# Optimization experiments

Hardware: AMD Instinct MI355X
Metric: run time of the kernel (lower is better)

## Reference

```python
import jax, jax.numpy as jnp
import numpy as np

B, S, D, H = 2, 2048, 2048, 16
HD = D // H  # head dim = 128


def setup_inputs() -> dict:
    key = jax.random.key(0)
    ks = jax.random.split(key, 9)
    sc = 1.0 / np.sqrt(D)
    return {
        "hidden_states": jax.random.normal(ks[0], (B, S, D), jnp.float32),
        "Wq": jax.random.normal(ks[1], (D, D), jnp.float32) * sc,
        "bq": jax.random.normal(ks[2], (D,), jnp.float32) * 0.02,
        "Wk": jax.random.normal(ks[3], (D, D), jnp.float32) * sc,
        "bk": jax.random.normal(ks[4], (D,), jnp.float32) * 0.02,
        "Wv": jax.random.normal(ks[5], (D, D), jnp.float32) * sc,
        "bv": jax.random.normal(ks[6], (D,), jnp.float32) * 0.02,
        "Wo": jax.random.normal(ks[7], (D, D), jnp.float32) * sc,
        "bo": jax.random.normal(ks[8], (D,), jnp.float32) * 0.02,
    }


def _rotate_half(x):
    x1, x2 = jnp.split(x, 2, axis=-1)
    return jnp.concatenate((-x2, x1), axis=-1)


def reference(hidden_states, Wq, bq, Wk, bk, Wv, bv, Wo, bo):
    b, s, d = hidden_states.shape
    # QKV projections (torch Linear: x @ W.T + b)
    def proj(W, bias):
        y = jnp.einsum('bsd,ed->bse', hidden_states, W) + bias
        return y.reshape(b, s, H, HD).transpose(0, 2, 1, 3)  # [B,H,S,HD]
    q, k, v = proj(Wq, bq), proj(Wk, bk), proj(Wv, bv)

    # Rotary embedding tables
    inv_freq = 1.0 / (10000.0 ** (jnp.arange(0, HD, 2, dtype=jnp.float32) / HD))
    t = jnp.arange(s, dtype=jnp.float32)
    freqs = jnp.einsum('i,j->ij', t, inv_freq)          # [S, HD/2]
    emb = jnp.concatenate((freqs, freqs), axis=-1)       # [S, HD]
    cos_cached, sin_cached = jnp.cos(emb), jnp.sin(emb)
    # NOTE: source unpacks `sin, cos = rotary_emb(...)` while forward returns
    # (cos, sin) -> swap is intentional to match original math.
    sin_t, cos_t = cos_cached, sin_cached
    q = q * cos_t + _rotate_half(q) * sin_t
    k = k * cos_t + _rotate_half(k) * sin_t

    scores = jnp.einsum('bhsd,bhtd->bhst', q, k) / jnp.sqrt(jnp.float32(HD))
    probs = jax.nn.softmax(scores, axis=-1)
    ctx = jnp.einsum('bhst,bhtd->bhsd', probs, v)
    ctx = ctx.transpose(0, 2, 1, 3).reshape(b, s, d)
    return jnp.einsum('bsd,ed->bse', ctx, Wo) + bo
```

## Files before the change

### kernel.cpp

```cpp
#include <hip/hip_runtime.h>

constexpr int NH = 16;
constexpr int SEQ = 2048;
constexpr int DMODEL = 2048;
constexpr int HDIM = 128;
constexpr int NB = 2;
constexpr int MTOT = NB * SEQ;
constexpr long NEL = (long)NB * SEQ * DMODEL;
constexpr long WEL = (long)DMODEL * DMODEL;
constexpr size_t FUSED_WS = 2ul * (4 * NEL + 3 * WEL + 12288);

typedef __attribute__((ext_vector_type(8))) __bf16 bf16x8;
typedef __attribute__((ext_vector_type(4))) float f32x4;

__device__ __forceinline__ float bf2f(ushort u) {
  union { uint i; float f; } v; v.i = ((uint)u) << 16; return v.f;
}
__device__ __forceinline__ ushort f2bf(float f) {
  union { float f; uint i; } v; v.f = f;
  uint r = (v.i + 0x7FFFu + ((v.i >> 16) & 1u)) >> 16;
  return (ushort)r;
}
__device__ __forceinline__ ushort f2bf_rhu(float f) {
  union { float f; uint i; } v; v.f = f;
  return (ushort)((v.i + 0x8000u) >> 16);
}
__device__ __forceinline__ float fast_exp2(float x) {
#if __has_builtin(__builtin_amdgcn_exp2f)
  return __builtin_amdgcn_exp2f(x);
#else
  float r;
  asm volatile("v_exp_f32 %0, %1\n\ts_nop 0" : "=v"(r) : "v"(x));
  return r;
#endif
}

__global__ __launch_bounds__(256) void conv_f32_bf16(
    const float* __restrict__ s, ushort* __restrict__ d, int n4) {
  const int i = blockIdx.x * 256 + threadIdx.x;
  if (i < n4) {
    const float4 v = ((const float4*)s)[i];
    ushort4 o;
    o.x = f2bf(v.x); o.y = f2bf(v.y); o.z = f2bf(v.z); o.w = f2bf(v.w);
    ((ushort4*)d)[i] = o;
  }
}

__global__ __launch_bounds__(256) void bias_cat(
    const float* __restrict__ a, const float* __restrict__ b,
    const float* __restrict__ c, float* __restrict__ o) {
  const int i = blockIdx.x * 256 + threadIdx.x;
  o[i] = (i < 2048) ? a[i] : (i < 4096) ? b[i - 2048] : c[i - 4096];
}

#define GLDS(src, dst)                                              \
  __builtin_amdgcn_global_load_lds(                                 \
      (const __attribute__((address_space(1))) void*)(src),         \
      (__attribute__((address_space(3))) void*)(dst), 16, 0, 0)

#define STG_A(d, kt) do {                                           \
    const ushort* _s = gA + (long)(kt) * 64;                        \
    ushort* _d = smem + (d) * 8192 + w * 512;                       \
    GLDS(_s, _d);                                                   \
    GLDS(_s + 64 * (long)K, _d + 4096);                             \
  } while (0)

#define STG_B0(d, kt) do {                                          \
    const ushort* _s = gB + (long)(kt) * 64;                        \
    ushort* _d = smem + 16384 + (d) * 16384 + w * 512;              \
    GLDS(_s, _d);                                                   \
    GLDS(_s + 64 * (long)K, _d + 4096);                             \
  } while (0)

#define STG_B1(d, kt) do {                                          \
    const ushort* _s = gB + 128 * (long)K + (long)(kt) * 64;        \
    ushort* _d = smem + 16384 + (d) * 16384 + 8192 + w * 512;       \
    GLDS(_s, _d);                                                   \
    GLDS(_s + 64 * (long)K, _d + 4096);                             \
  } while (0)

#define LDAF(d) do {                                                \
    const ushort* _p = smem + (d) * 8192 + (wm * 64 + l16) * 64;    \
    _Pragma("unroll")                                               \
    for (int _i = 0; _i < 4; _i++) {                                \
      afr[_i][0] = *(const bf16x8*)(_p + _i * 1024 + sw0);          \
      afr[_i][1] = *(const bf16x8*)(_p + _i * 1024 + sw1);          \
    }                                                               \
  } while (0)

#define LDBF(d, nh) do {                                            \
    const ushort* _p = smem + 16384 + (d) * 16384 +                 \
                       ((nh) * 128 + wn * 32 + l16) * 64;           \
    _Pragma("unroll")                                               \
    for (int _j = 0; _j < 2; _j++) {                                \
      bfr[nh][_j][0] = *(const bf16x8*)(_p + _j * 1024 + sw0);      \
      bfr[nh][_j][1] = *(const bf16x8*)(_p + _j * 1024 + sw1);      \
    }                                                               \
  } while (0)

#define MMAP(nh) do {                                               \
    __builtin_amdgcn_s_setprio(1);                                  \
    _Pragma("unroll")                                               \
    for (int _i = 0; _i < 4; _i++)                                  \
      _Pragma("unroll")                                             \
      for (int _j = 0; _j < 2; _j++) {                              \
        acc[_i][(nh) * 2 + _j] = __builtin_amdgcn_mfma_f32_16x16x32_bf16( \
            afr[_i][0], bfr[nh][_j][0], acc[_i][(nh) * 2 + _j], 0, 0, 0); \
        acc[_i][(nh) * 2 + _j] = __builtin_amdgcn_mfma_f32_16x16x32_bf16( \
            afr[_i][1], bfr[nh][_j][1], acc[_i][(nh) * 2 + _j], 0, 0, 0); \
      }                                                             \
    __builtin_amdgcn_s_setprio(0);                                  \
  } while (0)

#define BARX() __builtin_amdgcn_s_barrier()
#define WAITV(n) asm volatile("s_waitcnt vmcnt(" #n ")" ::: "memory")
#define WAITL() asm volatile("s_waitcnt lgkmcnt(0)" ::: "memory")

template <int MODE>
__global__ __launch_bounds__(512, 2) void gemm128(
    const ushort* __restrict__ A, const ushort* __restrict__ Bw,
    const float* __restrict__ bias, void* __restrict__ Cv,
    int M, int N, int K) {
  __shared__ __align__(16) ushort smem[49152];
  const int tid = threadIdx.x;
  const int w = tid >> 6, lane = tid & 63;
  const int quad = lane >> 4, l16 = lane & 15;
  const int wm = w >> 2, wn = w & 3;
  const int nbm = M >> 7, nbn = N >> 8;
  const int rm = nbm >> 1, rn = nbn >> 2;
  const int xcd = blockIdx.x & 7, loc = blockIdx.x >> 3;
  const int bm = (xcd >> 2) * rm + (loc % rm);
  const int bn = (xcd & 3) * rn + (loc / rm);
  const int m0 = bm << 7, n0 = bn << 8;
  const int KT = K >> 6;

  const int srow = tid >> 3;
  const int scol = (((tid & 7) ^ ((tid >> 3) & 7)) << 3);
  const ushort* gA = A + (long)(m0 + srow) * K + scol;
  const ushort* gB = Bw + (long)(n0 + srow) * K + scol;
  const int sw0 = ((quad ^ (l16 & 7)) << 3);
  const int sw1 = (((4 + quad) ^ (l16 & 7)) << 3);

  f32x4 acc[4][4] = {};
  bf16x8 afr[4][2];
  bf16x8 bfr[2][2][2];

  STG_B1(0, 0);
  STG_A(0, 0); STG_B0(0, 0);
  STG_A(1, 1); STG_B0(1, 1);
  WAITV(4);
  BARX();
  LDAF(0); LDBF(0, 0);
  WAITL();
  BARX();

  for (int t = 0; t < KT; t++) {
    const int d = t & 1, nd = d ^ 1;
    const int c1 = (t + 1 < KT) ? t + 1 : 0;
    const int c2 = (t + 2 < KT) ? t + 2 : (t + 2 - KT);
    STG_B1(nd, c1);
    STG_A(d, c2);
    WAITV(8);
    BARX();
    WAITL();
    MMAP(0);
    LDBF(d, 1);
    BARX();
    STG_B0(d, c2);
    WAITV(6);
    BARX();
    WAITL();
    MMAP(1);
    LDAF(nd); LDBF(nd, 0);
    BARX();
  }

#pragma unroll
  for (int i = 0; i < 4; i++) {
    const int rbase = m0 + wm * 64 + i * 16 + quad * 4;
#pragma unroll
    for (int nh = 0; nh < 2; nh++)
#pragma unroll
      for (int j = 0; j < 2; j++) {
        const int col = n0 + nh * 128 + wn * 32 + j * 16 + l16;
        const float bv = bias[col];
#pragma unroll
        for (int r = 0; r < 4; r++) {
          const int row = rbase + r;
          const float v = acc[i][nh * 2 + j][r] + bv;
          if (MODE == 0) {
            ((float*)Cv)[(long)row * N + col] = v;
          } else {
            const int b = row >> 11, s = row & (SEQ - 1);
            const int h = (col >> 7) & 15, hd = col & (HDIM - 1);
            const long off = (long)(col >> 11) * NEL +
                ((long)(b * NH + h) * SEQ + s) * HDIM + hd;
            ((ushort*)Cv)[off] = f2bf(v);
          }
        }
      }
  }
}

__global__ __launch_bounds__(256) void rope_qk(ushort* Q, ushort* Kt) {
  const int gid = blockIdx.x * 256 + threadIdx.x;
  const int n = gid & 4194303;
  const bool isK = (gid >= 4194304);
  ushort* ptr = isK ? Kt : Q;
  const float qs = isK ? 1.0f : 0.12751743f;
  const int p = n & 63;
  const int s = (n >> 6) & (SEQ - 1);
  const int bh = n >> 17;
  const long idx = (long)bh * (SEQ * HDIM) + (long)s * HDIM + p;
  const float invf_rev =
      fast_exp2(-(float)p * 0.2076205059304601f) * 0.15915494309189535f;
  float rev = (float)s * invf_rev;
  rev -= floorf(rev);
  const float sn = __builtin_amdgcn_sinf(rev);
  const float cs = __builtin_amdgcn_cosf(rev);
  const float x1 = bf2f(ptr[idx]);
  const float x2 = bf2f(ptr[idx + 64]);
  ptr[idx]      = f2bf((x1 * sn - x2 * cs) * qs);
  ptr[idx + 64] = f2bf((x2 * sn + x1 * cs) * qs);
}

__global__ __launch_bounds__(256) void transpose_v(const ushort* __restrict__ V,
                                                   ushort* __restrict__ VT) {
  __shared__ ushort lT[64 * 65];
  const int bh = blockIdx.x >> 6;
  const int rem = blockIdx.x & 63;
  const int t0 = (rem >> 1) << 6, d0 = (rem & 1) << 6;
  const ushort* vb = V + (long)bh * (SEQ * HDIM);
  ushort* ob = VT + (long)bh * (SEQ * HDIM);
  const int tid = threadIdx.x;
#pragma unroll
  for (int it = 0; it < 16; it++) {
    const int idx = it * 256 + tid;
    const int r = idx >> 6, c = idx & 63;
    lT[c * 65 + r] = vb[(long)(t0 + r) * HDIM + d0 + c];
  }
  __syncthreads();
#pragma unroll
  for (int it = 0; it < 16; it++) {
    const int idx = it * 256 + tid;
    const int r = idx >> 6, c = idx & 63;
    ob[(long)(d0 + r) * SEQ + t0 + c] = lT[r * 65 + c];
  }
}

__global__ __launch_bounds__(256, 2) void attn(const ushort* __restrict__ Q,
                                               const ushort* __restrict__ Kp,
                                               const ushort* __restrict__ VT,
                                               ushort* __restrict__ ctx) {
  __shared__ __align__(16) ushort smem[40960];
  const int tid = threadIdx.x;
  const int wave = tid >> 6, lane = tid & 63;
  const int quad = lane >> 4, l16 = lane & 15;
  const int xcd = blockIdx.x & 7, loc = blockIdx.x >> 3;
  const int bh = xcd * 4 + (loc >> 5), qt = loc & 31;
  const long hb = (long)bh * (SEQ * HDIM);
  const int b = bh >> 4, h = bh & 15;
  const int qh = wave & 1, th = wave >> 1;
  ushort* myP = smem + 35840 + wave * (32 * 40);

  bf16x8 qa[2][4];
#pragma unroll
  for (int qq = 0; qq < 2; qq++)
#pragma unroll
    for (int c = 0; c < 4; c++)
      qa[qq][c] = *(const bf16x8*)(
          Q + hb + (long)(qt * 64 + qh * 32 + qq * 16 + l16) * HDIM +
          c * 32 + (quad << 3));

  f32x4 o[2][8] = {};
  f32x4 lacc[2] = {};
  bf16x8 ones;
#pragma unroll
  for (int i = 0; i < 8; i++) ones[i] = (__bf16)1.0f;

  const ushort* kSrc = Kp + hb + (long)(tid >> 4) * HDIM + (tid & 15) * 8;
  const ushort* vSrc = VT + hb + (long)(tid >> 3) * SEQ + (tid & 7) * 8;
  const int kOff = (tid >> 4) * 136 + (tid & 15) * 8;
  const int vOff = (tid >> 3) * 72 + (tid & 7) * 8;

  {
    bf16x8 kR[4], vR[4];
#pragma unroll
    for (int it = 0; it < 4; it++) {
      kR[it] = *(const bf16x8*)(kSrc + (long)it * (16 * HDIM));
      vR[it] = *(const bf16x8*)(vSrc + (long)it * (32 * SEQ));
    }
    kSrc += 64 * HDIM; vSrc += 64;
#pragma unroll
    for (int it = 0; it < 4; it++) {
      *(bf16x8*)(smem + kOff + it * (16 * 136)) = kR[it];
      *(bf16x8*)(smem + 17408 + vOff + it * (32 * 72)) = vR[it];
    }
  }
  __syncthreads();

  for (int t0 = 0; t0 < SEQ; t0 += 64) {
    const int cur = (t0 >> 6) & 1;
    ushort* cK = cur ? smem + 8704 : smem;
    ushort* cV = cur ? smem + 26624 : smem + 17408;
    ushort* nK = cur ? smem : smem + 8704;
    ushort* nV = cur ? smem + 17408 : smem + 26624;
    const bool more = (t0 + 64 < SEQ);

    bf16x8 kR[4], vR[4];
    if (more) {
#pragma unroll
      for (int it = 0; it < 4; it++) {
        kR[it] = *(const bf16x8*)(kSrc + (long)it * (16 * HDIM));
        vR[it] = *(const bf16x8*)(vSrc + (long)it * (32 * SEQ));
      }
      kSrc += 64 * HDIM; vSrc += 64;
    }

    const ushort* kRow = cK + (th * 32 + l16) * 136 + (quad << 3);
    f32x4 st[2][2] = {};
    __builtin_amdgcn_s_setprio(1);
#pragma unroll
    for (int kc = 0; kc < 4; kc++)
#pragma unroll
      for (int tt = 0; tt < 2; tt++) {
        const bf16x8 ka = *(const bf16x8*)(kRow + tt * (16 * 136) + kc * 32);
#pragma unroll
        for (int qq = 0; qq < 2; qq++)
          st[tt][qq] = __builtin_amdgcn_mfma_f32_16x16x32_bf16(
              ka, qa[qq][kc], st[tt][qq], 0, 0, 0);
      }
    __builtin_amdgcn_s_setprio(0);

    ushort* pW = myP + l16 * 40 + (quad << 2);
#pragma unroll
    for (int qq = 0; qq < 2; qq++)
#pragma unroll
      for (int tt = 0; tt < 2; tt++) {
        ushort4 pk;
        pk.x = f2bf_rhu(fast_exp2(st[tt][qq][0]));
        pk.y = f2bf_rhu(fast_exp2(st[tt][qq][1]));
        pk.z = f2bf_rhu(fast_exp2(st[tt][qq][2]));
        pk.w = f2bf_rhu(fast_exp2(st[tt][qq][3]));
        *(ushort4*)(pW + qq * (16 * 40) + tt * 16) = pk;
      }
    WAITL();
    __builtin_amdgcn_sched_barrier(0);

    const ushort* pRow = myP + l16 * 40 + (quad << 3);
    const ushort* vRow = cV + l16 * 72 + th * 32 + (quad << 3);
    bf16x8 pa[2];
    __builtin_amdgcn_s_setprio(1);
#pragma unroll
    for (int qq = 0; qq < 2; qq++) {
      pa[qq] = *(const bf16x8*)(pRow + qq * (16 * 40));
      lacc[qq] = __builtin_amdgcn_mfma_f32_16x16x32_bf16(
          pa[qq], ones, lacc[qq], 0, 0, 0);
    }
#pragma unroll
    for (int nt = 0; nt < 8; nt++) {
      const bf16x8 vb = *(const bf16x8*)(vRow + nt * (16 * 72));
#pragma unroll
      for (int qq = 0; qq < 2; qq++)
        o[qq][nt] = __builtin_amdgcn_mfma_f32_16x16x32_bf16(
            pa[qq], vb, o[qq][nt], 0, 0, 0);
    }
    __builtin_amdgcn_s_setprio(0);

    if (more) {
#pragma unroll
      for (int it = 0; it < 4; it++) {
        *(bf16x8*)(nK + kOff + it * (16 * 136)) = kR[it];
        *(bf16x8*)(nV + vOff + it * (32 * 72)) = vR[it];
      }
    }
    __syncthreads();
  }

  float* mb = (float*)smem;
  if (wave >= 2) {
    float* p = mb + ((wave - 2) * 64 + lane) * 73;
#pragma unroll
    for (int qq = 0; qq < 2; qq++) {
#pragma unroll
      for (int nt = 0; nt < 8; nt++)
#pragma unroll
        for (int r = 0; r < 4; r++) p[qq * 32 + nt * 4 + r] = o[qq][nt][r];
#pragma unroll
      for (int r = 0; r < 4; r++) p[64 + qq * 4 + r] = lacc[qq][r];
    }
  }
  __syncthreads();
  if (wave < 2) {
    const float* p = mb + (wave * 64 + lane) * 73;
#pragma unroll
    for (int qq = 0; qq < 2; qq++) {
#pragma unroll
      for (int nt = 0; nt < 8; nt++)
#pragma unroll
        for (int r = 0; r < 4; r++) o[qq][nt][r] += p[qq * 32 + nt * 4 + r];
#pragma unroll
      for (int r = 0; r < 4; r++) lacc[qq][r] += p[64 + qq * 4 + r];
    }
#pragma unroll
    for (int qq = 0; qq < 2; qq++)
#pragma unroll
      for (int r = 0; r < 4; r++) {
        const float inv = 1.0f / lacc[qq][r];
        const int s = qt * 64 + qh * 32 + qq * 16 + quad * 4 + r;
        const long base = ((long)(b * SEQ + s)) * DMODEL + h * HDIM;
#pragma unroll
        for (int nt = 0; nt < 8; nt++)
          ctx[base + nt * 16 + l16] = f2bf(o[qq][nt][r] * inv);
      }
  }
}

extern "C" void kernel_launch(void* const* d_in, const int* in_sizes, int n_in,
                              void* d_out, int out_size, void* d_ws, size_t ws_size,
                              hipStream_t stream) {
  const float* hid = (const float*)d_in[0];
  const float* Wq = (const float*)d_in[1];
  const float* bq = (const float*)d_in[2];
  const float* Wk = (const float*)d_in[3];
  const float* bk = (const float*)d_in[4];
  const float* Wv = (const float*)d_in[5];
  const float* bv = (const float*)d_in[6];
  const float* Wo = (const float*)d_in[7];
  const float* bo = (const float*)d_in[8];
  float* out = (float*)d_out;
  ushort* ws = (ushort*)d_ws;

  ushort* qw   = ws;
  ushort* kw   = ws + NEL;
  ushort* vw   = ws + 2 * NEL;
  ushort* hidB = ws + 3 * NEL;
  ushort* wB   = ws + 4 * NEL;

  dim3 blk(256);
  dim3 blkG(512);
  conv_f32_bf16<<<(int)(NEL / 4 / 256), blk, 0, stream>>>(hid, hidB, NEL / 4);

  if (ws_size >= FUSED_WS) {
    conv_f32_bf16<<<(int)(WEL / 4 / 256), blk, 0, stream>>>(Wq, wB, WEL / 4);
    conv_f32_bf16<<<(int)(WEL / 4 / 256), blk, 0, stream>>>(Wk, wB + WEL, WEL / 4);
    conv_f32_bf16<<<(int)(WEL / 4 / 256), blk, 0, stream>>>(Wv, wB + 2 * WEL, WEL / 4);
    float* bc = (float*)(wB + 3 * WEL);
    bias_cat<<<24, blk, 0, stream>>>(bq, bk, bv, bc);
    gemm128<1><<<768, blkG, 0, stream>>>(hidB, wB, bc, qw, MTOT, 3 * DMODEL, DMODEL);
  } else {
    conv_f32_bf16<<<(int)(WEL / 4 / 256), blk, 0, stream>>>(Wq, wB, WEL / 4);
    gemm128<1><<<256, blkG, 0, stream>>>(hidB, wB, bq, qw, MTOT, DMODEL, DMODEL);
    conv_f32_bf16<<<(int)(WEL / 4 / 256), blk, 0, stream>>>(Wk, wB, WEL / 4);
    gemm128<1><<<256, blkG, 0, stream>>>(hidB, wB, bk, kw, MTOT, DMODEL, DMODEL);
    conv_f32_bf16<<<(int)(WEL / 4 / 256), blk, 0, stream>>>(Wv, wB, WEL / 4);
    gemm128<1><<<256, blkG, 0, stream>>>(hidB, wB, bv, vw, MTOT, DMODEL, DMODEL);
  }

  rope_qk<<<32768, blk, 0, stream>>>(qw, kw);

  ushort* vtw = hidB;
  transpose_v<<<2048, blk, 0, stream>>>(vw, vtw);

  ushort* cw = vw;
  attn<<<1024, blk, 0, stream>>>(qw, kw, vtw, cw);

  conv_f32_bf16<<<(int)(WEL / 4 / 256), blk, 0, stream>>>(Wo, wB, WEL / 4);
  gemm128<0><<<256, blkG, 0, stream>>>(cw, wB, bo, out, MTOT, DMODEL, DMODEL);
}
```

Measured before the change: 423.1 us.

## Add 128x384-tile GEMM kernel for fused QKV projection

Adds a new gemm384 kernel that computes a 128x384 output tile per block, staging three 128-column B sub-tiles through a 64 KB shared-memory pipeline. The fused QKV projection now launches 512 blocks of it instead of 768 blocks of the 128x256 kernel. The larger N tile is meant to reuse each A tile across more columns and cut global/LDS traffic for A. In exchange it uses more LDS and more accumulator registers per block, which may lower occupancy, and it relies on a more complex interleaved load/MMA schedule.

```diff
diff --git a/kernel.cpp b/kernel.cpp
--- a/kernel.cpp
+++ b/kernel.cpp
@@ -57,6 +57,162 @@
   __builtin_amdgcn_global_load_lds(                                 \
       (const __attribute__((address_space(1))) void*)(src),         \
       (__attribute__((address_space(3))) void*)(dst), 16, 0, 0)
+
+#define BARX() __builtin_amdgcn_s_barrier()
+#define WAITV(n) asm volatile("s_waitcnt vmcnt(" #n ")" ::: "memory")
+#define WAITL() asm volatile("s_waitcnt lgkmcnt(0)" ::: "memory")
+
+#define G3_STG_A(d, kt) do {                                        \
+    const ushort* _s = gA + (long)(kt) * 64;                        \
+    ushort* _d = smem + (d) * 8192 + w * 512;                       \
+    GLDS(_s, _d);                                                   \
+    GLDS(_s + 64 * (long)K, _d + 4096);                             \
+  } while (0)
+
+#define G3_STG_B(d, j, kt) do {                                     \
+    const ushort* _s = gB + (long)(j) * 128 * K + (long)(kt) * 64;  \
+    ushort* _d = smem + 16384 + (d) * 24576 + (j) * 8192 + w * 512; \
+    GLDS(_s, _d);                                                   \
+    GLDS(_s + 64 * (long)K, _d + 4096);                             \
+  } while (0)
+
+#define G3_LDA(d) do {                                              \
+    const ushort* _p = smem + (d) * 8192 + (wm * 64 + l16) * 64;    \
+    _Pragma("unroll")                                               \
+    for (int _i = 0; _i < 4; _i++) {                                \
+      afr[_i][0] = *(const bf16x8*)(_p + _i * 1024 + sw0);          \
+      afr[_i][1] = *(const bf16x8*)(_p + _i * 1024 + sw1);          \
+    }                                                               \
+  } while (0)
+
+#define G3_LDB(d, j, s) do {                                        \
+    const ushort* _p = smem + 16384 + (d) * 24576 + (j) * 8192 +    \
+                       (wn * 32 + l16) * 64;                        \
+    _Pragma("unroll")                                               \
+    for (int _j = 0; _j < 2; _j++) {                                \
+      bfr[s][_j][0] = *(const bf16x8*)(_p + _j * 1024 + sw0);       \
+      bfr[s][_j][1] = *(const bf16x8*)(_p + _j * 1024 + sw1);       \
+    }                                                               \
+  } while (0)
+
+#define G3_MMA(s, j) do {                                           \
+    __builtin_amdgcn_s_setprio(1);                                  \
+    _Pragma("unroll")                                               \
+    for (int _i = 0; _i < 4; _i++)                                  \
+      _Pragma("unroll")                                             \
+      for (int _j = 0; _j < 2; _j++) {                              \
+        acc[_i][(j) * 2 + _j] = __builtin_amdgcn_mfma_f32_16x16x32_bf16( \
+            afr[_i][0], bfr[s][_j][0], acc[_i][(j) * 2 + _j], 0, 0, 0);  \
+        acc[_i][(j) * 2 + _j] = __builtin_amdgcn_mfma_f32_16x16x32_bf16( \
+            afr[_i][1], bfr[s][_j][1], acc[_i][(j) * 2 + _j], 0, 0, 0);  \
+      }                                                             \
+    __builtin_amdgcn_s_setprio(0);                                  \
+  } while (0)
+
+template <int MODE>
+__global__ __launch_bounds__(512, 2) void gemm384(
+    const ushort* __restrict__ A, const ushort* __restrict__ Bw,
+    const float* __restrict__ bias, void* __restrict__ Cv,
+    int M, int N, int K) {
+  __shared__ __align__(16) ushort smem[65536];
+  const int tid = threadIdx.x;
+  const int w = tid >> 6, lane = tid & 63;
+  const int quad = lane >> 4, l16 = lane & 15;
+  const int wm = w >> 2, wn = w & 3;
+  const int nbm = M >> 7, nbn = N / 384;
+  const int rm = nbm >> 1, rn = nbn >> 2;
+  const int xcd = blockIdx.x & 7, loc = blockIdx.x >> 3;
+  const int bm = (xcd >> 2) * rm + (loc % rm);
+  const int bn = (xcd & 3) * rn + (loc / rm);
+  const int m0 = bm << 7, n0 = bn * 384;
+  const int KT = K >> 6;
+
+  const int srow = tid >> 3;
+  const int scol = (((tid & 7) ^ ((tid >> 3) & 7)) << 3);
+  const ushort* gA = A + (long)(m0 + srow) * K + scol;
+  const ushort* gB = Bw + (long)(n0 + srow) * K + scol;
+  const int sw0 = ((quad ^ (l16 & 7)) << 3);
+  const int sw1 = (((4 + quad) ^ (l16 & 7)) << 3);
+
+  f32x4 acc[4][6] = {};
+  bf16x8 afr[4][2];
+  bf16x8 bfr[2][2][2];
+
+  G3_STG_A(0, 0);
+  G3_STG_B(0, 0, 0); G3_STG_B(0, 1, 0); G3_STG_B(0, 2, 0);
+  G3_STG_A(1, 1);
+  G3_STG_B(1, 0, 1); G3_STG_B(1, 1, 1);
+  WAITV(10);
+  BARX();
+  G3_LDA(0); G3_LDB(0, 0, 0);
+  WAITL();
+  BARX();
+
+  for (int t = 0; t < KT; t += 2) {
+    const int e2 = (t + 2 < KT) ? t + 2 : 0;
+    const int e3 = (t + 3 < KT) ? t + 3 : 1;
+    G3_STG_B(1, 2, t + 1);
+    G3_STG_A(0, e2);
+    WAITV(10); BARX(); WAITL();
+    G3_MMA(0, 0);
+    G3_LDB(0, 1, 1);
+    BARX();
+    G3_STG_B(0, 0, e2);
+    BARX(); WAITL();
+    G3_MMA(1, 1);
+    G3_LDB(0, 2, 0);
+    BARX();
+    G3_STG_B(0, 1, e2);
+    WAITV(10); BARX(); WAITL();
+    G3_MMA(0, 2);
+    G3_LDA(1);
+    G3_LDB(1, 0, 1);
+    BARX();
+    G3_STG_B(0, 2, e2);
+    G3_STG_A(1, e3);
+    WAITV(10); BARX(); WAITL();
+    G3_MMA(1, 0);
+    G3_LDB(1, 1, 0);
+    BARX();
+    G3_STG_B(1, 0, e3);
+    BARX(); WAITL();
+    G3_MMA(0, 1);
+    G3_LDB(1, 2, 1);
+    BARX();
+    G3_STG_B(1, 1, e3);
+    WAITV(10); BARX(); WAITL();
+    G3_MMA(1, 2);
+    G3_LDA(0);
+    G3_LDB(0, 0, 0);
+    BARX();
+  }
+
+#pragma unroll
+  for (int i = 0; i < 4; i++) {
+    const int rbase = m0 + wm * 64 + i * 16 + quad * 4;
+#pragma unroll
+    for (int jt = 0; jt < 3; jt++)
+#pragma unroll
+      for (int j = 0; j < 2; j++) {
+        const int col = n0 + jt * 128 + wn * 32 + j * 16 + l16;
+        const float bv = bias[col];
+#pragma unroll
+        for (int r = 0; r < 4; r++) {
+          const int row = rbase + r;
+          const float v = acc[i][jt * 2 + j][r] + bv;
+          if (MODE == 0) {
+            ((float*)Cv)[(long)row * N + col] = v;
+          } else {
+            const int b = row >> 11, s = row & (SEQ - 1);
+            const int h = (col >> 7) & 15, hd = col & (HDIM - 1);
+            const long off = (long)(col >> 11) * NEL +
+                ((long)(b * NH + h) * SEQ + s) * HDIM + hd;
+            ((ushort*)Cv)[off] = f2bf(v);
+          }
+        }
+      }
+  }
+}
 
 #define STG_A(d, kt) do {                                           \
     const ushort* _s = gA + (long)(kt) * 64;                        \
@@ -111,10 +267,6 @@
       }                                                             \
     __builtin_amdgcn_s_setprio(0);                                  \
   } while (0)
-
-#define BARX() __builtin_amdgcn_s_barrier()
-#define WAITV(n) asm volatile("s_waitcnt vmcnt(" #n ")" ::: "memory")
-#define WAITL() asm volatile("s_waitcnt lgkmcnt(0)" ::: "memory")
 
 template <int MODE>
 __global__ __launch_bounds__(512, 2) void gemm128(
@@ -447,7 +599,7 @@
     conv_f32_bf16<<<(int)(WEL / 4 / 256), blk, 0, stream>>>(Wv, wB + 2 * WEL, WEL / 4);
     float* bc = (float*)(wB + 3 * WEL);
     bias_cat<<<24, blk, 0, stream>>>(bq, bk, bv, bc);
-    gemm128<1><<<768, blkG, 0, stream>>>(hidB, wB, bc, qw, MTOT, 3 * DMODEL, DMODEL);
+    gemm384<1><<<512, blkG, 0, stream>>>(hidB, wB, bc, qw, MTOT, 3 * DMODEL, DMODEL);
   } else {
     conv_f32_bf16<<<(int)(WEL / 4 / 256), blk, 0, stream>>>(Wq, wB, WEL / 4);
     gemm128<1><<<256, blkG, 0, stream>>>(hidB, wB, bq, qw, MTOT, DMODEL, DMODEL);
```

Result: faster. 403.3 us (-4.7%).
